# Optimization experiments

Measured on AMD Instinct MI355X. Metric: run time of the kernel, lower is better.

The kernel has to match this reference:

```python
import jax, jax.numpy as jnp
import numpy as np

EMBED_DIM = 1024
HIDDEN_DIM = 1024
NUM_HEADS = 16
CONTEXT_DIM = 768
HEAD_DIM = EMBED_DIM // NUM_HEADS
SCALE = HEAD_DIM ** -0.5


def setup_inputs() -> dict:
    key = jax.random.key(0)
    ks = jax.random.split(key, 7)
    B, N, M = 4, 4096, 1024
    tokens = jax.random.normal(ks[0], (B, N, HIDDEN_DIM), dtype=jnp.float32)
    context = jax.random.normal(ks[1], (B, M, CONTEXT_DIM), dtype=jnp.float32)
    # Linear weights stored as [in, out] (transposed torch layout)
    Wq = jax.random.normal(ks[2], (HIDDEN_DIM, EMBED_DIM), dtype=jnp.float32) * (HIDDEN_DIM ** -0.5)
    Wk = jax.random.normal(ks[3], (CONTEXT_DIM, EMBED_DIM), dtype=jnp.float32) * (CONTEXT_DIM ** -0.5)
    Wv = jax.random.normal(ks[4], (CONTEXT_DIM, HIDDEN_DIM), dtype=jnp.float32) * (CONTEXT_DIM ** -0.5)
    Wo = jax.random.normal(ks[5], (HIDDEN_DIM, HIDDEN_DIM), dtype=jnp.float32) * (HIDDEN_DIM ** -0.5)
    bo = jax.random.normal(ks[6], (HIDDEN_DIM,), dtype=jnp.float32) * 0.01
    return {"tokens": tokens, "context": context, "Wq": Wq, "Wk": Wk, "Wv": Wv, "Wo": Wo, "bo": bo}


def _split_heads(x):
    # [b, n, h*d] -> [b, h, n, d]
    b, n, _ = x.shape
    return x.reshape(b, n, NUM_HEADS, -1).transpose(0, 2, 1, 3)


def reference(tokens, context, Wq, Wk, Wv, Wo, bo):
    Q = _split_heads(tokens @ Wq)    # [b, h, n, d]
    K = _split_heads(context @ Wk)   # [b, h, m, d]
    V = _split_heads(context @ Wv)   # [b, h, m, dv]
    scores = jnp.einsum('bhnd,bhmd->bhnm', Q, K) * SCALE
    attn = jax.nn.softmax(scores, axis=-1)
    out = jnp.einsum('bhnm,bhmd->bhnd', attn, V)          # [b, h, n, dv]
    b, h, n, d = out.shape
    out = out.transpose(0, 2, 1, 3).reshape(b, n, h * d)  # [b, n, hidden]
    return out @ Wo + bo
```

## Files before the change

### kernel.cpp

```cpp
#include <hip/hip_runtime.h>
#include <hip/hip_bf16.h>
#include <math.h>

typedef unsigned short ushort_t;
typedef __attribute__((ext_vector_type(8))) short short8;
typedef __attribute__((ext_vector_type(4))) short short4v;
typedef __attribute__((ext_vector_type(4))) float f32x4;

#define MFMA16(a, b, c) __builtin_amdgcn_mfma_f32_16x16x32_bf16((a), (b), (c), 0, 0, 0)

__device__ __forceinline__ short8 ld_s8(const void* p) { return *(const short8*)p; }

__device__ __forceinline__ ushort_t f2bf(float x) {
  __hip_bfloat16 h = __float2bfloat16(x);
  return *reinterpret_cast<ushort_t*>(&h);
}

__device__ __forceinline__ void wave_fence() {
  __builtin_amdgcn_fence(__ATOMIC_ACQ_REL, "wavefront");
}

__device__ __forceinline__ void async_ld16(const void* g, void* l) {
  __builtin_amdgcn_global_load_lds(
      (const __attribute__((address_space(1))) unsigned int*)g,
      (__attribute__((address_space(3))) unsigned int*)l, 16, 0, 0);
}

__global__ __launch_bounds__(256) void cvt_k(const float* __restrict__ src,
                                             ushort_t* __restrict__ dst, size_t n8) {
  const size_t i = (size_t)blockIdx.x * 256 + threadIdx.x;
  if (i >= n8) return;
  const size_t base = i * 8;
  const float4 a = ((const float4*)(src + base))[0];
  const float4 b = ((const float4*)(src + base))[1];
  short8 o;
  o[0] = (short)f2bf(a.x); o[1] = (short)f2bf(a.y);
  o[2] = (short)f2bf(a.z); o[3] = (short)f2bf(a.w);
  o[4] = (short)f2bf(b.x); o[5] = (short)f2bf(b.y);
  o[6] = (short)f2bf(b.z); o[7] = (short)f2bf(b.w);
  *(short8*)(dst + base) = o;
}

__global__ void transpose_cvt2_k(const float* __restrict__ s0, const float* __restrict__ s1,
                                 ushort_t* __restrict__ d0, ushort_t* __restrict__ d1,
                                 int R, int C) {
  __shared__ ushort_t tile[32][33];
  const float* src = blockIdx.z ? s1 : s0;
  ushort_t* dst = blockIdx.z ? d1 : d0;
  const int bx = blockIdx.x * 32, by = blockIdx.y * 32;
  const int tx = threadIdx.x, ty = threadIdx.y;
#pragma unroll
  for (int i = 0; i < 32; i += 8)
    tile[ty + i][tx] = f2bf(src[(size_t)(by + ty + i) * C + bx + tx]);
  __syncthreads();
#pragma unroll
  for (int i = 0; i < 32; i += 8)
    dst[(size_t)(bx + ty + i) * R + by + tx] = tile[tx][ty + i];
}

#define BM 128
#define BN 128
#define BK 32

__device__ __forceinline__ void st1(float* p, float v) { *p = v; }
__device__ __forceinline__ void st1(__hip_bfloat16* p, float v) { *p = __float2bfloat16(v); }

template <typename OutT>
__global__ __launch_bounds__(256) void gemm_bt(const ushort_t* __restrict__ A,
                                               const ushort_t* __restrict__ Bt,
                                               OutT* __restrict__ C,
                                               const float* __restrict__ bias,
                                               int M, int N, int K) {
  __shared__ __align__(16) ushort_t sA[BM * BK];
  __shared__ __align__(16) ushort_t sB[BN * BK];
  const int tid = threadIdx.x;
  const int lane = tid & 63, wave = tid >> 6;
  const int lr = lane & 15, quad = lane >> 4;
  const int m0 = blockIdx.y * BM, n0 = blockIdx.x * BN;
  const int wm = (wave >> 1) * 64, wn = (wave & 1) * 64;
  const ushort_t* Ag = A + (size_t)m0 * K;
  const ushort_t* Bg = Bt + (size_t)n0 * K;
  const int srow = tid >> 2, scol = (tid & 3) * 8;
  const int wb = (tid & 192) * 8;

  f32x4 acc[4][4] = {};

  for (int k0 = 0; k0 < K; k0 += BK) {
    async_ld16(Ag + (size_t)srow * K + (k0 + scol), sA + wb);
    async_ld16(Ag + (size_t)(srow + 64) * K + (k0 + scol), sA + 2048 + wb);
    async_ld16(Bg + (size_t)srow * K + (k0 + scol), sB + wb);
    async_ld16(Bg + (size_t)(srow + 64) * K + (k0 + scol), sB + 2048 + wb);
    __syncthreads();
    short8 af[4], bf[4];
#pragma unroll
    for (int t = 0; t < 4; ++t) {
      af[t] = ld_s8(sA + (wm + t * 16 + lr) * BK + quad * 8);
      bf[t] = ld_s8(sB + (wn + t * 16 + lr) * BK + quad * 8);
    }
#pragma unroll
    for (int tm = 0; tm < 4; ++tm)
#pragma unroll
      for (int tn = 0; tn < 4; ++tn)
        acc[tm][tn] = MFMA16(af[tm], bf[tn], acc[tm][tn]);
    __syncthreads();
  }

#pragma unroll
  for (int tm = 0; tm < 4; ++tm) {
    const int row = m0 + wm + tm * 16 + quad * 4;
#pragma unroll
    for (int tn = 0; tn < 4; ++tn) {
      const int col = n0 + wn + tn * 16 + lr;
      const float bv = bias ? bias[col] : 0.0f;
#pragma unroll
      for (int r = 0; r < 4; ++r)
        st1(&C[(size_t)(row + r) * N + col], acc[tm][tn][r] + bv);
    }
  }
}

__global__ __launch_bounds__(256) void kv_gemm(const ushort_t* __restrict__ A,
                                               const ushort_t* __restrict__ Bt,
                                               ushort_t* __restrict__ KVb,
                                               ushort_t* __restrict__ Vt) {
  const int K = 768;
  __shared__ __align__(16) ushort_t sA[BM * BK];
  __shared__ __align__(16) ushort_t sB[BN * BK];
  const int tid = threadIdx.x;
  const int lane = tid & 63, wave = tid >> 6;
  const int lr = lane & 15, quad = lane >> 4;
  const int m0 = blockIdx.y * BM, n0 = blockIdx.x * BN;
  const int wm = (wave >> 1) * 64, wn = (wave & 1) * 64;
  const ushort_t* Ag = A + (size_t)m0 * K;
  const ushort_t* Bg = Bt + (size_t)n0 * K;
  const int srow = tid >> 2, scol = (tid & 3) * 8;
  const int wb = (tid & 192) * 8;

  f32x4 acc[4][4] = {};

  for (int k0 = 0; k0 < K; k0 += BK) {
    async_ld16(Ag + (size_t)srow * K + (k0 + scol), sA + wb);
    async_ld16(Ag + (size_t)(srow + 64) * K + (k0 + scol), sA + 2048 + wb);
    async_ld16(Bg + (size_t)srow * K + (k0 + scol), sB + wb);
    async_ld16(Bg + (size_t)(srow + 64) * K + (k0 + scol), sB + 2048 + wb);
    __syncthreads();
    short8 af[4], bf[4];
#pragma unroll
    for (int t = 0; t < 4; ++t) {
      af[t] = ld_s8(sA + (wm + t * 16 + lr) * BK + quad * 8);
      bf[t] = ld_s8(sB + (wn + t * 16 + lr) * BK + quad * 8);
    }
#pragma unroll
    for (int tm = 0; tm < 4; ++tm)
#pragma unroll
      for (int tn = 0; tn < 4; ++tn)
        acc[tm][tn] = MFMA16(af[tm], bf[tn], acc[tm][tn]);
    __syncthreads();
  }

#pragma unroll
  for (int tm = 0; tm < 4; ++tm) {
    const int row = m0 + wm + tm * 16 + quad * 4;
    const int b = row >> 10, mloc = row & 1023;
#pragma unroll
    for (int tn = 0; tn < 4; ++tn) {
      const int col = n0 + wn + tn * 16 + lr;
      if (col < 1024) {
#pragma unroll
        for (int r = 0; r < 4; ++r)
          KVb[(size_t)(row + r) * 2048 + col] = f2bf(acc[tm][tn][r]);
      } else {
        ushort_t* vp = Vt + ((size_t)b * 1024 + (col - 1024)) * 1024 + mloc;
#pragma unroll
        for (int r = 0; r < 4; ++r)
          vp[r] = f2bf(acc[tm][tn][r]);
      }
    }
  }
}

__global__ __launch_bounds__(256) void attn_k(const ushort_t* __restrict__ Q,
                                              const ushort_t* __restrict__ KVb,
                                              const ushort_t* __restrict__ Vt,
                                              __hip_bfloat16* __restrict__ O) {
  __shared__ __align__(16) ushort_t sK[64 * 64];
  __shared__ __align__(16) ushort_t sV[64 * 64];
  __shared__ __align__(16) ushort_t sP[4 * 32 * 64];
  const int tid = threadIdx.x;
  const int lane = tid & 63, wave = tid >> 6;
  const int lr = lane & 15, quad = lane >> 4;
  const int b = blockIdx.z, h = blockIdx.y;
  const int q0 = blockIdx.x * 128 + wave * 32;
  const int key = (lr & 7) << 4;

  const ushort_t* Qg = Q + ((size_t)b * 4096 + q0 + lr) * 1024 + h * 64;
  short8 qf[2][2];
#pragma unroll
  for (int t = 0; t < 2; ++t) {
    qf[t][0] = ld_s8(Qg + (size_t)t * 16 * 1024 + quad * 8);
    qf[t][1] = ld_s8(Qg + (size_t)t * 16 * 1024 + 32 + quad * 8);
  }
  const ushort_t* Kg = KVb + (size_t)b * 1024 * 2048 + h * 64;
  const ushort_t* Vg = Vt + ((size_t)b * 1024 + h * 64) * 1024;

  const int srow = lane >> 3;
  const int scol = ((lane & 7) ^ srow) * 8;
  const ushort_t* k0 = Kg + (size_t)(wave * 8 + srow) * 2048 + scol;
  const ushort_t* v0 = Vg + (size_t)(wave * 8 + srow) * 1024 + scol;
  ushort_t* dK = sK + wave * 512;
  ushort_t* dV = sV + wave * 512;
  ushort_t* sPw = sP + wave * 2048;

  const float c1 = 0.125f * 1.44269504f;
  const float c2 = 16.0f * 1.44269504f;

  float lsum0 = 0.0f, lsum1 = 0.0f;
  f32x4 o0[4] = {}, o1[4] = {};

  for (int it = 0; it < 16; ++it) {
    __syncthreads();
    async_ld16(k0, dK);
    async_ld16(k0 + (size_t)32 * 2048, dK + 2048);
    async_ld16(v0, dV);
    async_ld16(v0 + (size_t)32 * 1024, dV + 2048);
    k0 += (size_t)64 * 2048;
    v0 += 64;
    __syncthreads();

    wave_fence();
#pragma unroll
    for (int nt = 0; nt < 4; ++nt) {
      const int krow = nt * 16 + lr;
      const short8 ka = ld_s8((const char*)sK + ((krow * 128 + quad * 16) ^ key));
      const short8 kb = ld_s8((const char*)sK + ((krow * 128 + 64 + quad * 16) ^ key));
#pragma unroll
      for (int t = 0; t < 2; ++t) {
        f32x4 z = {};
        z = MFMA16(ka, qf[t][0], z);
        z = MFMA16(kb, qf[t][1], z);
        short4v pk;
        float ls = 0.0f;
#pragma unroll
        for (int r = 0; r < 4; ++r) {
          const float p = __builtin_amdgcn_exp2f(fmaf(z[r], c1, -c2));
          ls += p;
          pk[r] = (short)f2bf(p);
        }
        if (t == 0) lsum0 += ls; else lsum1 += ls;
        *(short4v*)((char*)sPw +
                    (((t * 16 + lr) * 128 + nt * 32 + quad * 8) ^ key)) = pk;
      }
    }
    wave_fence();

#pragma unroll
    for (int ks = 0; ks < 2; ++ks) {
      const short8 p0 = ld_s8((const char*)sPw + ((lr * 128 + ks * 64 + quad * 16) ^ key));
      const short8 p1 = ld_s8((const char*)sPw + (((16 + lr) * 128 + ks * 64 + quad * 16) ^ key));
#pragma unroll
      for (int dt = 0; dt < 4; ++dt) {
        const short8 vv =
            ld_s8((const char*)sV + (((dt * 16 + lr) * 128 + ks * 64 + quad * 16) ^ key));
        o0[dt] = MFMA16(p0, vv, o0[dt]);
        o1[dt] = MFMA16(p1, vv, o1[dt]);
      }
    }
  }

#pragma unroll
  for (int t = 0; t < 2; ++t) {
    float l = t ? lsum1 : lsum0;
    l += __shfl_xor(l, 16);
    l += __shfl_xor(l, 32);
    const float rinv = 1.0f / l;
    const f32x4* oa = t ? o1 : o0;
    __hip_bfloat16* Og = O + ((size_t)b * 4096 + q0 + t * 16 + quad * 4) * 1024 + h * 64;
#pragma unroll
    for (int r = 0; r < 4; ++r) {
      const float rl = __shfl(rinv, quad * 4 + r);
#pragma unroll
      for (int dt = 0; dt < 4; ++dt)
        Og[(size_t)r * 1024 + dt * 16 + lr] = __float2bfloat16(oa[dt][r] * rl);
    }
  }
}

extern "C" void kernel_launch(void* const* d_in, const int* in_sizes, int n_in,
                              void* d_out, int out_size, void* d_ws, size_t ws_size,
                              hipStream_t stream) {
  (void)in_sizes; (void)n_in; (void)out_size; (void)ws_size;
  const float* tokens  = (const float*)d_in[0];
  const float* context = (const float*)d_in[1];
  const float* Wq = (const float*)d_in[2];
  const float* Wk = (const float*)d_in[3];
  const float* Wv = (const float*)d_in[4];
  const float* Wo = (const float*)d_in[5];
  const float* bo = (const float*)d_in[6];
  float* out = (float*)d_out;

  ushort_t* ws = (ushort_t*)d_ws;
  ushort_t* tokB = ws; ws += (size_t)16384 * 1024;
  ushort_t* ctxB = ws; ws += (size_t)4096 * 768;
  ushort_t* WqT  = ws; ws += (size_t)1024 * 1024;
  ushort_t* WkvT = ws; ws += (size_t)2048 * 768;
  ushort_t* WoT  = ws; ws += (size_t)1024 * 1024;
  ushort_t* Qb   = ws; ws += (size_t)16384 * 1024;
  ushort_t* KVb  = ws; ws += (size_t)4096 * 2048;
  ushort_t* Vt   = ws; ws += (size_t)4096 * 1024;
  ushort_t* Ab   = Qb;

  cvt_k<<<8192, 256, 0, stream>>>(tokens, tokB, (size_t)16384 * 1024 / 8);
  cvt_k<<<1536, 256, 0, stream>>>(context, ctxB, (size_t)4096 * 768 / 8);

  const dim3 tb(32, 8);
  transpose_cvt2_k<<<dim3(32, 32, 2), tb, 0, stream>>>(Wq, Wo, WqT, WoT, 1024, 1024);
  transpose_cvt2_k<<<dim3(32, 24, 2), tb, 0, stream>>>(Wk, Wv, WkvT, WkvT + (size_t)1024 * 768,
                                                       768, 1024);

  gemm_bt<__hip_bfloat16><<<dim3(8, 128), 256, 0, stream>>>(
      tokB, WqT, (__hip_bfloat16*)Qb, nullptr, 16384, 1024, 1024);
  kv_gemm<<<dim3(16, 32), 256, 0, stream>>>(ctxB, WkvT, KVb, Vt);

  attn_k<<<dim3(32, 16, 4), 256, 0, stream>>>(Qb, KVb, Vt, (__hip_bfloat16*)Ab);

  gemm_bt<float><<<dim3(8, 128), 256, 0, stream>>>(
      Ab, WoT, out, bo, 16384, 1024, 1024);
}
```

Before: 397.8 us.

## Double-buffer K/V tiles in attention and raise wave priority around MFMAs

The attention kernel now keeps two shared-memory buffers each for K and V. It prefetches the next 64-key tile with asynchronous global-to-LDS loads while computing on the current tile, so each iteration needs one barrier instead of two, and global load latency can overlap the QK^T, softmax and PV math. The MFMA sections are also wrapped in s_setprio to favour waves issuing matrix ops. The cost is twice the LDS for K/V, which may reduce occupancy, and correctness relies on the barrier waiting for the outstanding async loads.

New measurement: 400.9 us. About the same (+0.8%).

```diff
diff --git a/kernel.cpp b/kernel.cpp
--- a/kernel.cpp
+++ b/kernel.cpp
@@ -183,8 +183,8 @@
                                               const ushort_t* __restrict__ KVb,
                                               const ushort_t* __restrict__ Vt,
                                               __hip_bfloat16* __restrict__ O) {
-  __shared__ __align__(16) ushort_t sK[64 * 64];
-  __shared__ __align__(16) ushort_t sV[64 * 64];
+  __shared__ __align__(16) ushort_t sK[2][64 * 64];
+  __shared__ __align__(16) ushort_t sV[2][64 * 64];
   __shared__ __align__(16) ushort_t sP[4 * 32 * 64];
   const int tid = threadIdx.x;
   const int lane = tid & 63, wave = tid >> 6;
@@ -207,8 +207,6 @@
   const int scol = ((lane & 7) ^ srow) * 8;
   const ushort_t* k0 = Kg + (size_t)(wave * 8 + srow) * 2048 + scol;
   const ushort_t* v0 = Vg + (size_t)(wave * 8 + srow) * 1024 + scol;
-  ushort_t* dK = sK + wave * 512;
-  ushort_t* dV = sV + wave * 512;
   ushort_t* sPw = sP + wave * 2048;
 
   const float c1 = 0.125f * 1.44269504f;
@@ -217,27 +215,44 @@
   float lsum0 = 0.0f, lsum1 = 0.0f;
   f32x4 o0[4] = {}, o1[4] = {};
 
-  for (int it = 0; it < 16; ++it) {
-    __syncthreads();
+  {
+    ushort_t* dK = sK[0] + wave * 512;
+    ushort_t* dV = sV[0] + wave * 512;
     async_ld16(k0, dK);
     async_ld16(k0 + (size_t)32 * 2048, dK + 2048);
     async_ld16(v0, dV);
     async_ld16(v0 + (size_t)32 * 1024, dV + 2048);
-    k0 += (size_t)64 * 2048;
-    v0 += 64;
-    __syncthreads();
-
-    wave_fence();
+  }
+
+  for (int it = 0; it < 16; ++it) {
+    __syncthreads();
+
+    const ushort_t* cK = sK[it & 1];
+    const ushort_t* cV = sV[it & 1];
+
+    if (it < 15) {
+      k0 += (size_t)64 * 2048;
+      v0 += 64;
+      ushort_t* dK = sK[(it + 1) & 1] + wave * 512;
+      ushort_t* dV = sV[(it + 1) & 1] + wave * 512;
+      async_ld16(k0, dK);
+      async_ld16(k0 + (size_t)32 * 2048, dK + 2048);
+      async_ld16(v0, dV);
+      async_ld16(v0 + (size_t)32 * 1024, dV + 2048);
+    }
+
 #pragma unroll
     for (int nt = 0; nt < 4; ++nt) {
       const int krow = nt * 16 + lr;
-      const short8 ka = ld_s8((const char*)sK + ((krow * 128 + quad * 16) ^ key));
-      const short8 kb = ld_s8((const char*)sK + ((krow * 128 + 64 + quad * 16) ^ key));
+      const short8 ka = ld_s8((const char*)cK + ((krow * 128 + quad * 16) ^ key));
+      const short8 kb = ld_s8((const char*)cK + ((krow * 128 + 64 + quad * 16) ^ key));
 #pragma unroll
       for (int t = 0; t < 2; ++t) {
         f32x4 z = {};
+        __builtin_amdgcn_s_setprio(1);
         z = MFMA16(ka, qf[t][0], z);
         z = MFMA16(kb, qf[t][1], z);
+        __builtin_amdgcn_s_setprio(0);
         short4v pk;
         float ls = 0.0f;
 #pragma unroll
@@ -253,6 +268,7 @@
     }
     wave_fence();
 
+    __builtin_amdgcn_s_setprio(1);
 #pragma unroll
     for (int ks = 0; ks < 2; ++ks) {
       const short8 p0 = ld_s8((const char*)sPw + ((lr * 128 + ks * 64 + quad * 16) ^ key));
@@ -260,11 +276,13 @@
 #pragma unroll
       for (int dt = 0; dt < 4; ++dt) {
         const short8 vv =
-            ld_s8((const char*)sV + (((dt * 16 + lr) * 128 + ks * 64 + quad * 16) ^ key));
+            ld_s8((const char*)cV + (((dt * 16 + lr) * 128 + ks * 64 + quad * 16) ^ key));
         o0[dt] = MFMA16(p0, vv, o0[dt]);
         o1[dt] = MFMA16(p1, vv, o1[dt]);
       }
     }
+    __builtin_amdgcn_s_setprio(0);
+    wave_fence();
   }
 
 #pragma unroll
```

## Double-buffer attention K/V tiles, widen GEMM K-step, add XCD block swizzle

Applied to the files above, without the earlier changes.

The attention kernel now keeps two LDS buffers for K and V. The next tile's async global-to-LDS loads are issued while the current tile is being computed, and the PV MFMA section runs at raised wave priority. This aims to hide global load latency and cut barrier stalls in the main loop. Both GEMM kernels move from a K-step of 32 to 64 with two MFMA sub-steps per stage, which halves barrier count per unit of work. They also remap block IDs so neighbouring tiles land on the same XCD for better L2 reuse. The costs are more LDS use, which may lower occupancy, and possible new LDS bank conflicts from the 128-byte unswizzled GEMM rows.

New measurement: 381.9 us. 1.04x faster.

```diff
diff --git a/kernel.cpp b/kernel.cpp
--- a/kernel.cpp
+++ b/kernel.cpp
@@ -60,10 +60,17 @@
 
 #define BM 128
 #define BN 128
-#define BK 32
+#define BK 64
 
 __device__ __forceinline__ void st1(float* p, float v) { *p = v; }
 __device__ __forceinline__ void st1(__hip_bfloat16* p, float v) { *p = __float2bfloat16(v); }
+
+__device__ __forceinline__ int2 xcd_swz(int nx) {
+  const int id = blockIdx.y * gridDim.x + blockIdx.x;
+  const int cpx = (gridDim.x * gridDim.y) >> 3;
+  const int nid = (id & 7) * cpx + (id >> 3);
+  int2 r; r.x = nid % nx; r.y = nid / nx; return r;
+}
 
 template <typename OutT>
 __global__ __launch_bounds__(256) void gemm_bt(const ushort_t* __restrict__ A,
@@ -76,32 +83,39 @@
   const int tid = threadIdx.x;
   const int lane = tid & 63, wave = tid >> 6;
   const int lr = lane & 15, quad = lane >> 4;
-  const int m0 = blockIdx.y * BM, n0 = blockIdx.x * BN;
+  const int2 bid = xcd_swz(gridDim.x);
+  const int m0 = bid.y * BM, n0 = bid.x * BN;
   const int wm = (wave >> 1) * 64, wn = (wave & 1) * 64;
   const ushort_t* Ag = A + (size_t)m0 * K;
   const ushort_t* Bg = Bt + (size_t)n0 * K;
-  const int srow = tid >> 2, scol = (tid & 3) * 8;
+  const int srow = tid >> 3, scol = (tid & 7) * 8;
   const int wb = (tid & 192) * 8;
 
   f32x4 acc[4][4] = {};
 
   for (int k0 = 0; k0 < K; k0 += BK) {
-    async_ld16(Ag + (size_t)srow * K + (k0 + scol), sA + wb);
-    async_ld16(Ag + (size_t)(srow + 64) * K + (k0 + scol), sA + 2048 + wb);
-    async_ld16(Bg + (size_t)srow * K + (k0 + scol), sB + wb);
-    async_ld16(Bg + (size_t)(srow + 64) * K + (k0 + scol), sB + 2048 + wb);
-    __syncthreads();
-    short8 af[4], bf[4];
-#pragma unroll
-    for (int t = 0; t < 4; ++t) {
-      af[t] = ld_s8(sA + (wm + t * 16 + lr) * BK + quad * 8);
-      bf[t] = ld_s8(sB + (wn + t * 16 + lr) * BK + quad * 8);
-    }
-#pragma unroll
-    for (int tm = 0; tm < 4; ++tm)
-#pragma unroll
-      for (int tn = 0; tn < 4; ++tn)
-        acc[tm][tn] = MFMA16(af[tm], bf[tn], acc[tm][tn]);
+    const ushort_t* Ai = Ag + (size_t)srow * K + (k0 + scol);
+    const ushort_t* Bi = Bg + (size_t)srow * K + (k0 + scol);
+#pragma unroll
+    for (int r0 = 0; r0 < 4; ++r0) {
+      async_ld16(Ai + (size_t)(r0 * 32) * K, sA + r0 * 2048 + wb);
+      async_ld16(Bi + (size_t)(r0 * 32) * K, sB + r0 * 2048 + wb);
+    }
+    __syncthreads();
+#pragma unroll
+    for (int kk = 0; kk < 2; ++kk) {
+      short8 af[4], bf[4];
+#pragma unroll
+      for (int t = 0; t < 4; ++t) {
+        af[t] = ld_s8(sA + (wm + t * 16 + lr) * BK + kk * 32 + quad * 8);
+        bf[t] = ld_s8(sB + (wn + t * 16 + lr) * BK + kk * 32 + quad * 8);
+      }
+#pragma unroll
+      for (int tm = 0; tm < 4; ++tm)
+#pragma unroll
+        for (int tn = 0; tn < 4; ++tn)
+          acc[tm][tn] = MFMA16(af[tm], bf[tn], acc[tm][tn]);
+    }
     __syncthreads();
   }
 
@@ -129,32 +143,39 @@
   const int tid = threadIdx.x;
   const int lane = tid & 63, wave = tid >> 6;
   const int lr = lane & 15, quad = lane >> 4;
-  const int m0 = blockIdx.y * BM, n0 = blockIdx.x * BN;
+  const int2 bid = xcd_swz(gridDim.x);
+  const int m0 = bid.y * BM, n0 = bid.x * BN;
   const int wm = (wave >> 1) * 64, wn = (wave & 1) * 64;
   const ushort_t* Ag = A + (size_t)m0 * K;
   const ushort_t* Bg = Bt + (size_t)n0 * K;
-  const int srow = tid >> 2, scol = (tid & 3) * 8;
+  const int srow = tid >> 3, scol = (tid & 7) * 8;
   const int wb = (tid & 192) * 8;
 
   f32x4 acc[4][4] = {};
 
   for (int k0 = 0; k0 < K; k0 += BK) {
-    async_ld16(Ag + (size_t)srow * K + (k0 + scol), sA + wb);
-    async_ld16(Ag + (size_t)(srow + 64) * K + (k0 + scol), sA + 2048 + wb);
-    async_ld16(Bg + (size_t)srow * K + (k0 + scol), sB + wb);
-    async_ld16(Bg + (size_t)(srow + 64) * K + (k0 + scol), sB + 2048 + wb);
-    __syncthreads();
-    short8 af[4], bf[4];
-#pragma unroll
-    for (int t = 0; t < 4; ++t) {
-      af[t] = ld_s8(sA + (wm + t * 16 + lr) * BK + quad * 8);
-      bf[t] = ld_s8(sB + (wn + t * 16 + lr) * BK + quad * 8);
-    }
-#pragma unroll
-    for (int tm = 0; tm < 4; ++tm)
-#pragma unroll
-      for (int tn = 0; tn < 4; ++tn)
-        acc[tm][tn] = MFMA16(af[tm], bf[tn], acc[tm][tn]);
+    const ushort_t* Ai = Ag + (size_t)srow * K + (k0 + scol);
+    const ushort_t* Bi = Bg + (size_t)srow * K + (k0 + scol);
+#pragma unroll
+    for (int r0 = 0; r0 < 4; ++r0) {
+      async_ld16(Ai + (size_t)(r0 * 32) * K, sA + r0 * 2048 + wb);
+      async_ld16(Bi + (size_t)(r0 * 32) * K, sB + r0 * 2048 + wb);
+    }
+    __syncthreads();
+#pragma unroll
+    for (int kk = 0; kk < 2; ++kk) {
+      short8 af[4], bf[4];
+#pragma unroll
+      for (int t = 0; t < 4; ++t) {
+        af[t] = ld_s8(sA + (wm + t * 16 + lr) * BK + kk * 32 + quad * 8);
+        bf[t] = ld_s8(sB + (wn + t * 16 + lr) * BK + kk * 32 + quad * 8);
+      }
+#pragma unroll
+      for (int tm = 0; tm < 4; ++tm)
+#pragma unroll
+        for (int tn = 0; tn < 4; ++tn)
+          acc[tm][tn] = MFMA16(af[tm], bf[tn], acc[tm][tn]);
+    }
     __syncthreads();
   }
 
@@ -183,8 +204,10 @@
                                               const ushort_t* __restrict__ KVb,
                                               const ushort_t* __restrict__ Vt,
                                               __hip_bfloat16* __restrict__ O) {
-  __shared__ __align__(16) ushort_t sK[64 * 64];
-  __shared__ __align__(16) ushort_t sV[64 * 64];
+  __shared__ __align__(16) ushort_t sK0[64 * 64];
+  __shared__ __align__(16) ushort_t sK1[64 * 64];
+  __shared__ __align__(16) ushort_t sV0[64 * 64];
+  __shared__ __align__(16) ushort_t sV1[64 * 64];
   __shared__ __align__(16) ushort_t sP[4 * 32 * 64];
   const int tid = threadIdx.x;
   const int lane = tid & 63, wave = tid >> 6;
@@ -207,9 +230,11 @@
   const int scol = ((lane & 7) ^ srow) * 8;
   const ushort_t* k0 = Kg + (size_t)(wave * 8 + srow) * 2048 + scol;
   const ushort_t* v0 = Vg + (size_t)(wave * 8 + srow) * 1024 + scol;
-  ushort_t* dK = sK + wave * 512;
-  ushort_t* dV = sV + wave * 512;
-  ushort_t* sPw = sP + wave * 2048;
+  ushort_t* const dK0 = sK0 + wave * 512;
+  ushort_t* const dK1 = sK1 + wave * 512;
+  ushort_t* const dV0 = sV0 + wave * 512;
+  ushort_t* const dV1 = sV1 + wave * 512;
+  ushort_t* const sPw = sP + wave * 2048;
 
   const float c1 = 0.125f * 1.44269504f;
   const float c2 = 16.0f * 1.44269504f;
@@ -217,55 +242,66 @@
   float lsum0 = 0.0f, lsum1 = 0.0f;
   f32x4 o0[4] = {}, o1[4] = {};
 
-  for (int it = 0; it < 16; ++it) {
-    __syncthreads();
-    async_ld16(k0, dK);
-    async_ld16(k0 + (size_t)32 * 2048, dK + 2048);
-    async_ld16(v0, dV);
-    async_ld16(v0 + (size_t)32 * 1024, dV + 2048);
-    k0 += (size_t)64 * 2048;
-    v0 += 64;
-    __syncthreads();
-
-    wave_fence();
-#pragma unroll
-    for (int nt = 0; nt < 4; ++nt) {
-      const int krow = nt * 16 + lr;
-      const short8 ka = ld_s8((const char*)sK + ((krow * 128 + quad * 16) ^ key));
-      const short8 kb = ld_s8((const char*)sK + ((krow * 128 + 64 + quad * 16) ^ key));
-#pragma unroll
-      for (int t = 0; t < 2; ++t) {
-        f32x4 z = {};
-        z = MFMA16(ka, qf[t][0], z);
-        z = MFMA16(kb, qf[t][1], z);
-        short4v pk;
-        float ls = 0.0f;
-#pragma unroll
-        for (int r = 0; r < 4; ++r) {
-          const float p = __builtin_amdgcn_exp2f(fmaf(z[r], c1, -c2));
-          ls += p;
-          pk[r] = (short)f2bf(p);
-        }
-        if (t == 0) lsum0 += ls; else lsum1 += ls;
-        *(short4v*)((char*)sPw +
-                    (((t * 16 + lr) * 128 + nt * 32 + quad * 8) ^ key)) = pk;
-      }
-    }
-    wave_fence();
-
-#pragma unroll
-    for (int ks = 0; ks < 2; ++ks) {
-      const short8 p0 = ld_s8((const char*)sPw + ((lr * 128 + ks * 64 + quad * 16) ^ key));
-      const short8 p1 = ld_s8((const char*)sPw + (((16 + lr) * 128 + ks * 64 + quad * 16) ^ key));
-#pragma unroll
-      for (int dt = 0; dt < 4; ++dt) {
-        const short8 vv =
-            ld_s8((const char*)sV + (((dt * 16 + lr) * 128 + ks * 64 + quad * 16) ^ key));
-        o0[dt] = MFMA16(p0, vv, o0[dt]);
-        o1[dt] = MFMA16(p1, vv, o1[dt]);
-      }
-    }
-  }
+#define STAGE(dK, dV)                                  \
+  do {                                                 \
+    async_ld16(k0, (dK));                              \
+    async_ld16(k0 + (size_t)32 * 2048, (dK) + 2048);   \
+    async_ld16(v0, (dV));                              \
+    async_ld16(v0 + (size_t)32 * 1024, (dV) + 2048);   \
+    k0 += (size_t)64 * 2048;                           \
+    v0 += 64;                                          \
+  } while (0)
+
+#define COMPUTE(cK, cV)                                                                   \
+  do {                                                                                    \
+    _Pragma("unroll") for (int nt = 0; nt < 4; ++nt) {                                    \
+      const int krow = nt * 16 + lr;                                                      \
+      const short8 ka = ld_s8((const char*)(cK) + ((krow * 128 + quad * 16) ^ key));      \
+      const short8 kb = ld_s8((const char*)(cK) + ((krow * 128 + 64 + quad * 16) ^ key)); \
+      _Pragma("unroll") for (int t = 0; t < 2; ++t) {                                     \
+        f32x4 z = {};                                                                     \
+        z = MFMA16(ka, qf[t][0], z);                                                      \
+        z = MFMA16(kb, qf[t][1], z);                                                      \
+        short4v pk;                                                                       \
+        float ls = 0.0f;                                                                  \
+        _Pragma("unroll") for (int r = 0; r < 4; ++r) {                                   \
+          const float p = __builtin_amdgcn_exp2f(fmaf(z[r], c1, -c2));                    \
+          ls += p;                                                                        \
+          pk[r] = (short)f2bf(p);                                                         \
+        }                                                                                 \
+        if (t == 0) lsum0 += ls; else lsum1 += ls;                                        \
+        *(short4v*)((char*)sPw + (((t * 16 + lr) * 128 + nt * 32 + quad * 8) ^ key)) = pk;\
+      }                                                                                   \
+    }                                                                                     \
+    wave_fence();                                                                         \
+    __builtin_amdgcn_s_setprio(1);                                                        \
+    _Pragma("unroll") for (int ks = 0; ks < 2; ++ks) {                                    \
+      const short8 p0 = ld_s8((const char*)sPw + ((lr * 128 + ks * 64 + quad * 16) ^ key)); \
+      const short8 p1 = ld_s8((const char*)sPw + (((16 + lr) * 128 + ks * 64 + quad * 16) ^ key)); \
+      _Pragma("unroll") for (int dt = 0; dt < 4; ++dt) {                                  \
+        const short8 vv =                                                                 \
+            ld_s8((const char*)(cV) + (((dt * 16 + lr) * 128 + ks * 64 + quad * 16) ^ key)); \
+        o0[dt] = MFMA16(p0, vv, o0[dt]);                                                  \
+        o1[dt] = MFMA16(p1, vv, o1[dt]);                                                  \
+      }                                                                                   \
+    }                                                                                     \
+    __builtin_amdgcn_s_setprio(0);                                                        \
+    wave_fence();                                                                         \
+  } while (0)
+
+  STAGE(dK0, dV0);
+
+#pragma unroll 1
+  for (int it2 = 0; it2 < 8; ++it2) {
+    __syncthreads();
+    STAGE(dK1, dV1);
+    COMPUTE(sK0, sV0);
+    __syncthreads();
+    if (it2 < 7) STAGE(dK0, dV0);
+    COMPUTE(sK1, sV1);
+  }
+#undef STAGE
+#undef COMPUTE
 
 #pragma unroll
   for (int t = 0; t < 2; ++t) {
```
